# Performance work log

Measured on AMD Instinct MI355X. Metric: run time of the kernel, lower is better.

Reference implementation:

```python
import jax, jax.numpy as jnp
import numpy as np

B = 64          # number of graphs
N_PER = 512     # nodes per graph (equal counts required by final view)
D = 64          # hidden_channels
R = 4           # channel-attention reduction


def setup_inputs() -> dict:
    key = jax.random.key(0)
    k1, k2, k3, k4, k5 = jax.random.split(key, 5)
    M = B * N_PER
    x = jax.random.normal(k1, (M, D), dtype=jnp.float32)
    batch = jnp.repeat(jnp.arange(B, dtype=jnp.int32), N_PER)  # sorted, equal segments
    # channel_attention mode=1 params (torch Linear: y = x @ W.T + b)
    s1 = 1.0 / np.sqrt(D)
    s2 = 1.0 / np.sqrt(D // R)
    W1 = jax.random.uniform(k2, (D // R, D), jnp.float32, -s1, s1)
    b1 = jax.random.uniform(k3, (D // R,), jnp.float32, -s1, s1)
    W2 = jax.random.uniform(k4, (D, D // R), jnp.float32, -s2, s2)
    b2 = jax.random.uniform(k5, (D,), jnp.float32, -s2, s2)
    return {"x": x, "batch": batch, "W1": W1, "b1": b1, "W2": W2, "b2": b2}


def reference(x, batch, W1, b1, W2, b2):
    M, d = x.shape
    # ---- channel_attention (mode=1, sigmoid gate) ----
    sums = jax.ops.segment_sum(x, batch, num_segments=B)                 # [B, D]
    cnts = jax.ops.segment_sum(jnp.ones((M, 1), x.dtype), batch, num_segments=B)
    gap = sums / cnts                                                    # scatter_mean
    h = jax.nn.leaky_relu(gap @ W1.T + b1, negative_slope=0.01)
    imp = jax.nn.sigmoid(h @ W2.T + b2)                                  # [B, D]
    xg = x * imp[batch]                                                  # repeat_interleave broadcast
    # ---- per-node outer product + triu vectorization ----
    # einsum('ik,kj->kij', x.T, x)[k] = outer(x[k], x[k]); take upper triangle (incl diag)
    iu0, iu1 = jnp.triu_indices(d)                                       # row-major triu order
    triu = xg[:, iu0] * xg[:, iu1]                                       # [M, D(D+1)/2]
    return triu.reshape(B, -1)
```

## Files before the change

### kernel.cpp

```cpp
#include <hip/hip_runtime.h>
#include <math.h>

#define NB_GRAPHS 64
#define NPER 512
#define DCH 64
#define DR 16
#define TRIU4 520

__global__ __launch_bounds__(512) void gap_mlp_kernel(
    const float* __restrict__ x,
    const float* __restrict__ W1, const float* __restrict__ b1,
    const float* __restrict__ W2, const float* __restrict__ b2,
    float* __restrict__ imp)
{
    __shared__ float part[8 * 64];
    __shared__ float sgap[64];
    __shared__ float sh[16];

    const int b   = blockIdx.x;
    const int tid = threadIdx.x;
    const int d   = tid & 63;
    const int rg  = tid >> 6;

    const float* xb = x + (size_t)b * NPER * DCH;
    float s = 0.f;
    #pragma unroll
    for (int r = 0; r < 64; ++r) {
        s += xb[(size_t)(rg * 64 + r) * DCH + d];
    }
    part[rg * 64 + d] = s;
    __syncthreads();

    if (tid < 64) {
        float t = 0.f;
        #pragma unroll
        for (int g = 0; g < 8; ++g) t += part[g * 64 + tid];
        sgap[tid] = t * (1.0f / 512.0f);
    }
    __syncthreads();

    if (tid < DR) {
        float acc = b1[tid];
        #pragma unroll
        for (int k = 0; k < 64; ++k) acc += sgap[k] * W1[tid * 64 + k];
        sh[tid] = acc >= 0.f ? acc : 0.01f * acc;
    }
    __syncthreads();

    if (tid < 64) {
        float acc = b2[tid];
        #pragma unroll
        for (int j = 0; j < DR; ++j) acc += sh[j] * W2[tid * DR + j];
        imp[b * 64 + tid] = 1.0f / (1.0f + expf(-acc));
    }
}

__global__ __launch_bounds__(256) void sop_kernel(
    const float* __restrict__ x,
    const float* __restrict__ imp,
    float* __restrict__ out)
{
    __shared__ unsigned int tI[TRIU4];
    __shared__ unsigned int tJ[TRIU4];
    __shared__ float v[4][64];

    const int tid = threadIdx.x;

    for (int t4 = tid; t4 < TRIU4; t4 += 256) {
        unsigned int pi = 0, pj = 0;
        #pragma unroll
        for (int e = 0; e < 4; ++e) {
            int tt = t4 * 4 + e;
            int ii = 0, rem = tt;
            while (rem >= 64 - ii) { rem -= 64 - ii; ++ii; }
            int jj = ii + rem;
            pi |= (unsigned int)ii << (8 * e);
            pj |= (unsigned int)jj << (8 * e);
        }
        tI[t4] = pi;
        tJ[t4] = pj;
    }
    __syncthreads();

    const int w    = tid >> 6;
    const int lane = tid & 63;
    float* vw = v[w];

    for (int it = 0; it < 4; ++it) {
        const int m = blockIdx.x * 16 + it * 4 + w;
        const int b = m >> 9;
        const float val = x[(size_t)m * DCH + lane] * imp[(b << 6) + lane];

        __syncthreads();
        vw[lane] = val;
        __syncthreads();

        float4* ob = reinterpret_cast<float4*>(out) + (size_t)m * TRIU4;
        #pragma unroll
        for (int k = 0; k < 9; ++k) {
            int t4 = k * 64 + lane;
            if (t4 < TRIU4) {
                unsigned int pi = tI[t4];
                unsigned int pj = tJ[t4];
                float4 o;
                o.x = vw[pi & 255u]         * vw[pj & 255u];
                o.y = vw[(pi >> 8) & 255u]  * vw[(pj >> 8) & 255u];
                o.z = vw[(pi >> 16) & 255u] * vw[(pj >> 16) & 255u];
                o.w = vw[pi >> 24]          * vw[pj >> 24];
                ob[t4] = o;
            }
        }
    }
}

extern "C" void kernel_launch(void* const* d_in, const int* in_sizes, int n_in,
                              void* d_out, int out_size, void* d_ws, size_t ws_size,
                              hipStream_t stream) {
    const float* x  = (const float*)d_in[0];
    const float* W1 = (const float*)d_in[2];
    const float* b1 = (const float*)d_in[3];
    const float* W2 = (const float*)d_in[4];
    const float* b2 = (const float*)d_in[5];
    float* out = (float*)d_out;
    float* imp = (float*)d_ws;

    gap_mlp_kernel<<<NB_GRAPHS, 512, 0, stream>>>(x, W1, b1, W2, b2, imp);
    sop_kernel<<<(NB_GRAPHS * NPER) / 16, 256, 0, stream>>>(x, imp, out);
}
```

Baseline: 305.3 us.

## Vectorize loads, hoist triu tables to registers, preload node vectors with swizzled byte offsets

The GAP kernel now reads x as float4 with 32 row groups, and the partial-sum reduction grows to match. The SOP kernel loads all four nodes per wave in a single float4 read before the main loop and stores them in a swizzled shared layout addressed by byte offsets. This removes the two per-iteration barriers and the scalar global loads. The triu index tables are moved into registers once instead of being re-read from shared memory every iteration. The cost is higher register pressure and an index encoding that is harder to follow.

New measurement: 302.6 us. About the same (-0.9%).

```diff
diff --git a/kernel.cpp b/kernel.cpp
--- a/kernel.cpp
+++ b/kernel.cpp
@@ -13,45 +13,49 @@
     const float* __restrict__ W2, const float* __restrict__ b2,
     float* __restrict__ imp)
 {
-    __shared__ float part[8 * 64];
+    __shared__ float part[32][64];
     __shared__ float sgap[64];
     __shared__ float sh[16];
 
     const int b   = blockIdx.x;
     const int tid = threadIdx.x;
-    const int d   = tid & 63;
-    const int rg  = tid >> 6;
+    const int c4  = tid & 15;
+    const int rg  = tid >> 4;
 
-    const float* xb = x + (size_t)b * NPER * DCH;
-    float s = 0.f;
+    const float4* xb = reinterpret_cast<const float4*>(x + (size_t)b * NPER * DCH);
+    float4 acc = {0.f, 0.f, 0.f, 0.f};
     #pragma unroll
-    for (int r = 0; r < 64; ++r) {
-        s += xb[(size_t)(rg * 64 + r) * DCH + d];
+    for (int k = 0; k < 16; ++k) {
+        float4 t = xb[(size_t)(rg + 32 * k) * 16 + c4];
+        acc.x += t.x; acc.y += t.y; acc.z += t.z; acc.w += t.w;
     }
-    part[rg * 64 + d] = s;
+    part[rg][c4 * 4 + 0] = acc.x;
+    part[rg][c4 * 4 + 1] = acc.y;
+    part[rg][c4 * 4 + 2] = acc.z;
+    part[rg][c4 * 4 + 3] = acc.w;
     __syncthreads();
 
     if (tid < 64) {
         float t = 0.f;
         #pragma unroll
-        for (int g = 0; g < 8; ++g) t += part[g * 64 + tid];
+        for (int g = 0; g < 32; ++g) t += part[g][tid];
         sgap[tid] = t * (1.0f / 512.0f);
     }
     __syncthreads();
 
     if (tid < DR) {
-        float acc = b1[tid];
+        float a = b1[tid];
         #pragma unroll
-        for (int k = 0; k < 64; ++k) acc += sgap[k] * W1[tid * 64 + k];
-        sh[tid] = acc >= 0.f ? acc : 0.01f * acc;
+        for (int k = 0; k < 64; ++k) a += sgap[k] * W1[tid * 64 + k];
+        sh[tid] = a >= 0.f ? a : 0.01f * a;
     }
     __syncthreads();
 
     if (tid < 64) {
-        float acc = b2[tid];
+        float a = b2[tid];
         #pragma unroll
-        for (int j = 0; j < DR; ++j) acc += sh[j] * W2[tid * DR + j];
-        imp[b * 64 + tid] = 1.0f / (1.0f + expf(-acc));
+        for (int j = 0; j < DR; ++j) a += sh[j] * W2[tid * DR + j];
+        imp[b * 64 + tid] = 1.0f / (1.0f + expf(-a));
     }
 }
 
@@ -62,9 +66,13 @@
 {
     __shared__ unsigned int tI[TRIU4];
     __shared__ unsigned int tJ[TRIU4];
-    __shared__ float v[4][64];
+    __shared__ float v[4][4][64];
 
-    const int tid = threadIdx.x;
+    const int tid  = threadIdx.x;
+    const int w    = tid >> 6;
+    const int lane = tid & 63;
+    const int m0   = blockIdx.x * 16;
+    const int b    = m0 >> 9;
 
     for (int t4 = tid; t4 < TRIU4; t4 += 256) {
         unsigned int pi = 0, pj = 0;
@@ -74,40 +82,56 @@
             int ii = 0, rem = tt;
             while (rem >= 64 - ii) { rem -= 64 - ii; ++ii; }
             int jj = ii + rem;
-            pi |= (unsigned int)ii << (8 * e);
-            pj |= (unsigned int)jj << (8 * e);
+            unsigned int ai = ((((unsigned)ii & 3u) << 4) | ((unsigned)ii >> 2)) << 2;
+            unsigned int aj = ((((unsigned)jj & 3u) << 4) | ((unsigned)jj >> 2)) << 2;
+            pi |= ai << (8 * e);
+            pj |= aj << (8 * e);
         }
         tI[t4] = pi;
         tJ[t4] = pj;
     }
+
+    const float4 xv  = reinterpret_cast<const float4*>(x + (size_t)(m0 + 4 * w) * DCH)[lane];
+    const float4 iv4 = reinterpret_cast<const float4*>(imp + ((size_t)b << 6))[lane & 15];
+    {
+        const int n  = lane >> 4;
+        const int cc = lane & 15;
+        float* vn = &v[w][n][0];
+        vn[0 * 16 + cc] = xv.x * iv4.x;
+        vn[1 * 16 + cc] = xv.y * iv4.y;
+        vn[2 * 16 + cc] = xv.z * iv4.z;
+        vn[3 * 16 + cc] = xv.w * iv4.w;
+    }
+
     __syncthreads();
 
-    const int w    = tid >> 6;
-    const int lane = tid & 63;
-    float* vw = v[w];
+    unsigned int ti[9], tj[9];
+    #pragma unroll
+    for (int k = 0; k < 9; ++k) {
+        int t4 = k * 64 + lane;
+        ti[k] = (t4 < TRIU4) ? tI[t4] : 0u;
+        tj[k] = (t4 < TRIU4) ? tJ[t4] : 0u;
+    }
 
+    #pragma unroll
     for (int it = 0; it < 4; ++it) {
-        const int m = blockIdx.x * 16 + it * 4 + w;
-        const int b = m >> 9;
-        const float val = x[(size_t)m * DCH + lane] * imp[(b << 6) + lane];
-
-        __syncthreads();
-        vw[lane] = val;
-        __syncthreads();
-
+        const int m = m0 + 4 * w + it;
+        const char* vb = reinterpret_cast<const char*>(&v[w][it][0]);
         float4* ob = reinterpret_cast<float4*>(out) + (size_t)m * TRIU4;
         #pragma unroll
         for (int k = 0; k < 9; ++k) {
-            int t4 = k * 64 + lane;
-            if (t4 < TRIU4) {
-                unsigned int pi = tI[t4];
-                unsigned int pj = tJ[t4];
+            if (k < 8 || lane < 8) {
+                const unsigned int pi = ti[k], pj = tj[k];
                 float4 o;
-                o.x = vw[pi & 255u]         * vw[pj & 255u];
-                o.y = vw[(pi >> 8) & 255u]  * vw[(pj >> 8) & 255u];
-                o.z = vw[(pi >> 16) & 255u] * vw[(pj >> 16) & 255u];
-                o.w = vw[pi >> 24]          * vw[pj >> 24];
-                ob[t4] = o;
+                o.x = *reinterpret_cast<const float*>(vb + (pi & 255u))
+                    * *reinterpret_cast<const float*>(vb + (pj & 255u));
+                o.y = *reinterpret_cast<const float*>(vb + ((pi >> 8) & 255u))
+                    * *reinterpret_cast<const float*>(vb + ((pj >> 8) & 255u));
+                o.z = *reinterpret_cast<const float*>(vb + ((pi >> 16) & 255u))
+                    * *reinterpret_cast<const float*>(vb + ((pj >> 16) & 255u));
+                o.w = *reinterpret_cast<const float*>(vb + (pi >> 24))
+                    * *reinterpret_cast<const float*>(vb + (pj >> 24));
+                ob[k * 64 + lane] = o;
             }
         }
     }
```
